# Optimization experiments

Hardware: AMD Instinct MI355X
Metric: run time of the kernel (lower is better)

## Reference

```python
import jax, jax.numpy as jnp
import numpy as np

NUM_USERS = 50000
NUM_ITEMS = 20000
N_NODES = NUM_USERS + NUM_ITEMS
D = 128           # embedding_dim
HEADS = 4
E_RAW = 400000    # raw edges (< 500000 threshold -> no subsampling)
BATCH = 16384
NEG_SLOPE = 0.2   # PyG GATConv leaky_relu slope
LN_EPS = 1e-5


def segment_softmax(logits, seg, num_segments):
    # PyG softmax: exp(x - max_per_segment) / (sum_per_segment + 1e-16)
    m = jax.ops.segment_max(logits, seg, num_segments=num_segments)
    m = jnp.where(jnp.isfinite(m), m, 0.0)  # empty segments
    e = jnp.exp(logits - m[seg])
    s = jax.ops.segment_sum(e, seg, num_segments=num_segments)
    return e / (s[seg] + 1e-16)


def gat_conv(x, src, dst, W, att_s, att_d, bias, heads):
    # PyG GATConv (concat=True): h = x @ W reshaped to [N, H, C]
    N = x.shape[0]
    HC = W.shape[1]
    C = HC // heads
    h = (x @ W).reshape(N, heads, C)
    a_s = (h * att_s).sum(-1)            # [N, H]
    a_d = (h * att_d).sum(-1)            # [N, H]
    logits = jax.nn.leaky_relu(a_s[src] + a_d[dst], NEG_SLOPE)  # [E, H]
    alpha = segment_softmax(logits, dst, N)                      # [E, H]
    msg = h[src] * alpha[:, :, None]                             # [E, H, C]
    out = jax.ops.segment_sum(msg, dst, num_segments=N)         # [N, H, C]
    return out.reshape(N, HC) + bias


def layer_norm(x, g, b):
    mu = x.mean(-1, keepdims=True)
    var = ((x - mu) ** 2).mean(-1, keepdims=True)
    return (x - mu) * jax.lax.rsqrt(var + LN_EPS) * g + b


def setup_inputs() -> dict:
    key = jax.random.key(0)
    ks = jax.random.split(key, 24)
    s = 0.05
    # graph: random edges with no self-loops, then append PyG self-loops
    src = jax.random.randint(ks[0], (E_RAW,), 0, N_NODES)
    off = jax.random.randint(ks[1], (E_RAW,), 1, N_NODES)
    dst = (src + off) % N_NODES
    loops = jnp.arange(N_NODES)
    edge_index = jnp.stack([jnp.concatenate([src, loops]),
                            jnp.concatenate([dst, loops])]).astype(jnp.int64)
    H1 = D // HEADS  # per-head dim for layers 0,1
    inp = {
        "user_indices": jax.random.randint(ks[2], (BATCH,), 0, NUM_USERS),
        "item_indices": jax.random.randint(ks[3], (BATCH,), 0, NUM_ITEMS),
        "edge_index": edge_index,
        "user_table": jax.random.normal(ks[4], (NUM_USERS, D)) * s,
        "item_table": jax.random.normal(ks[5], (NUM_ITEMS, D)) * s,
        # layer 0: GATConv(D, D//heads, heads)
        "W0": jax.random.normal(ks[6], (D, HEADS * H1)) * s,
        "as0": jax.random.normal(ks[7], (1, HEADS, H1)) * s,
        "ad0": jax.random.normal(ks[8], (1, HEADS, H1)) * s,
        "bb0": jnp.zeros((HEADS * H1,)),
        # layer 1: same shape
        "W1": jax.random.normal(ks[9], (D, HEADS * H1)) * s,
        "as1": jax.random.normal(ks[10], (1, HEADS, H1)) * s,
        "ad1": jax.random.normal(ks[11], (1, HEADS, H1)) * s,
        "bb1": jnp.zeros((HEADS * H1,)),
        # layer 2: GATConv(D, D) with heads=1
        "W2": jax.random.normal(ks[12], (D, D)) * s,
        "as2": jax.random.normal(ks[13], (1, 1, D)) * s,
        "ad2": jax.random.normal(ks[14], (1, 1, D)) * s,
        "bb2": jnp.zeros((D,)),
        "ln_g": jnp.ones((D,)),
        "ln_b": jnp.zeros((D,)),
        # prediction MLP
        "mw1": jax.random.normal(ks[15], (2 * D, D)) * s,
        "mb1": jnp.zeros((D,)),
        "mw2": jax.random.normal(ks[16], (D, D // 2)) * s,
        "mb2": jnp.zeros((D // 2,)),
        "mw3": jax.random.normal(ks[17], (D // 2, 1)) * s,
        "mb3": jnp.zeros((1,)),
    }
    return inp


def reference(user_indices, item_indices, edge_index, user_table, item_table,
              W0, as0, ad0, bb0, W1, as1, ad1, bb1, W2, as2, ad2, bb2,
              ln_g, ln_b, mw1, mb1, mw2, mb2, mw3, mb3):
    src, dst = edge_index[0], edge_index[1]
    x = jnp.concatenate([user_table, item_table], axis=0)  # [N, D]
    layers = [(W0, as0, ad0, bb0, HEADS), (W1, as1, ad1, bb1, HEADS),
              (W2, as2, ad2, bb2, 1)]
    for i, (W, a_s, a_d, bb, h) in enumerate(layers):
        x_new = jax.nn.elu(gat_conv(x, src, dst, W, a_s, a_d, bb, h))
        x = x_new + x if i > 0 else x_new  # residual (shapes always match here)
        x = layer_norm(x, ln_g, ln_b)
    user_emb = x[user_indices]
    item_emb = x[item_indices + NUM_USERS]
    combined = jnp.concatenate([user_emb, item_emb], axis=1)  # [B, 2D]
    hmlp = jax.nn.relu(combined @ mw1 + mb1)
    hmlp = jax.nn.relu(hmlp @ mw2 + mb2)
    logits = (hmlp @ mw3 + mb3)[:, 0]
    return jax.nn.sigmoid(logits)
```

## Files before the change

kernel.cpp:

```cpp
#include <hip/hip_runtime.h>
#include <hip/hip_bf16.h>

#define D128 128
#define NEG_SLOPE 0.2f

typedef __attribute__((ext_vector_type(8))) short bf16x8;
typedef __attribute__((ext_vector_type(4))) float f32x4;

__device__ inline float bf2f(unsigned short u) {
    return __uint_as_float(((unsigned)u) << 16);
}
__device__ inline unsigned short f2bf(float f) {
    unsigned u = __float_as_uint(f);
    unsigned r = (u + 0x7fffu + ((u >> 16) & 1u)) >> 16;
    return (unsigned short)r;
}

__global__ void zero_int_kernel(int* __restrict__ p, int n) {
    int i = blockIdx.x * blockDim.x + threadIdx.x;
    if (i < n) p[i] = 0;
}

__global__ void count_kernel(const int* __restrict__ dst, int E, int* __restrict__ cnt) {
    int e = blockIdx.x * blockDim.x + threadIdx.x;
    if (e < E) atomicAdd(&cnt[dst[e]], 1);
}

#define SB 256
#define SCAN_CHUNK 2048

__global__ __launch_bounds__(SB) void scan_local_kernel(const int* __restrict__ cnt,
                                                        int* __restrict__ off,
                                                        int* __restrict__ partials, int N) {
    __shared__ int lds[SB];
    const int b = blockIdx.x;
    const int t = threadIdx.x;
    const int base = b * SCAN_CHUNK + t * 8;
    int v[8];
    int s = 0;
#pragma unroll
    for (int j = 0; j < 8; ++j) {
        int i = base + j;
        v[j] = (i < N) ? cnt[i] : 0;
        s += v[j];
    }
    lds[t] = s;
    __syncthreads();
    for (int d = 1; d < SB; d <<= 1) {
        int y = (t >= d) ? lds[t - d] : 0;
        __syncthreads();
        lds[t] += y;
        __syncthreads();
    }
    int pref = lds[t] - s;
#pragma unroll
    for (int j = 0; j < 8; ++j) {
        int i = base + j;
        if (i < N) off[i] = pref;
        pref += v[j];
    }
    if (t == SB - 1) partials[b] = lds[t];
}

__global__ __launch_bounds__(64) void scan_partials_kernel(int* __restrict__ partials,
                                                           int* __restrict__ pp, int NB,
                                                           int* __restrict__ off, int N) {
    __shared__ int lds[64];
    int t = threadIdx.x;
    int v = (t < NB) ? partials[t] : 0;
    lds[t] = v;
    __syncthreads();
    for (int d = 1; d < 64; d <<= 1) {
        int y = (t >= d) ? lds[t - d] : 0;
        __syncthreads();
        lds[t] += y;
        __syncthreads();
    }
    pp[t] = lds[t] - v;
    if (t == 63) off[N] = lds[63];
}

__global__ void scan_add_kernel(int* __restrict__ off, int* __restrict__ cur,
                                const int* __restrict__ pp, int N) {
    int i = blockIdx.x * blockDim.x + threadIdx.x;
    if (i < N) {
        int o = off[i] + pp[i / SCAN_CHUNK];
        off[i] = o;
        cur[i] = o;
    }
}

__global__ void fill_kernel(const int* __restrict__ src, const int* __restrict__ dst, int E,
                            int* __restrict__ cur, int* __restrict__ csr_src,
                            int* __restrict__ csr_dst) {
    int e = blockIdx.x * blockDim.x + threadIdx.x;
    if (e < E) {
        int d = dst[e];
        int p = atomicAdd(&cur[d], 1);
        csr_src[p] = src[e];
        csr_dst[p] = d;
    }
}

__global__ __launch_bounds__(256) void wrepack3_kernel(const float* __restrict__ W0,
                                                       const float* __restrict__ W1,
                                                       const float* __restrict__ W2,
                                                       unsigned short* __restrict__ wb0,
                                                       unsigned short* __restrict__ wb1,
                                                       unsigned short* __restrict__ wb2) {
    const float* W = (blockIdx.y == 0) ? W0 : (blockIdx.y == 1) ? W1 : W2;
    unsigned short* Wb = (blockIdx.y == 0) ? wb0 : (blockIdx.y == 1) ? wb1 : wb2;
    int i = blockIdx.x * 256 + threadIdx.x;
    if (i >= 16384) return;
    int j = i & 7;
    int l = (i >> 3) & 63;
    int kk = (i >> 9) & 3;
    int ct = i >> 11;
    int k = kk * 32 + ((l >> 4) & 3) * 8 + j;
    int c = ct * 16 + (l & 15);
    float w = W[k * 128 + c];
    unsigned short hi = f2bf(w);
    unsigned short lo = f2bf(w - bf2f(hi));
    Wb[i] = hi;
    Wb[16384 + i] = lo;
}

__global__ __launch_bounds__(256) void wrepack_mlp_kernel(const float* __restrict__ mw1,
                                                          unsigned short* __restrict__ w1f,
                                                          const float* __restrict__ mw2,
                                                          unsigned short* __restrict__ w2f) {
    const int y = blockIdx.y;
    const float* W = y ? mw2 : mw1;
    unsigned short* Wf = y ? w2f : w1f;
    const int K = y ? 128 : 256, C = y ? 64 : 128;
    int total = K * C;
    int i = blockIdx.x * 256 + threadIdx.x;
    if (i >= total) return;
    int j = i & 7;
    int l = (i >> 3) & 63;
    int kkct = i >> 9;
    int KK = K >> 5;
    int kk = kkct % KK;
    int ct = kkct / KK;
    int k = kk * 32 + (l >> 4) * 8 + j;
    int c = ct * 16 + (l & 15);
    Wf[i] = f2bf(W[k * C + c]);
}

template <int H, bool SPLIT>
__global__ __launch_bounds__(512) void gemm_mfma_kernel(const float* __restrict__ X0,
                                                        const float* __restrict__ X1, int split,
                                                        const unsigned short* __restrict__ Wb,
                                                        const float* __restrict__ att_s,
                                                        const float* __restrict__ att_d,
                                                        unsigned short* __restrict__ hb,
                                                        float* __restrict__ a_s,
                                                        float* __restrict__ a_d, int N) {
    __shared__ unsigned short wlds[32768];
    const int t = threadIdx.x;
    const int lane = t & 63;
    const int wave = t >> 6;
    const int row0 = blockIdx.x * 128 + wave * 16;

    for (int i = t; i < 4096; i += 512)
        ((int4*)wlds)[i] = ((const int4*)Wb)[i];

    const int lr = lane & 15;
    const int lk = lane >> 4;

    int arow = row0 + lr;
    if (arow >= N) arow = N - 1;
    const float* xrow;
    if (SPLIT)
        xrow = (arow < split) ? &X0[(size_t)arow * 128] : &X1[(size_t)(arow - split) * 128];
    else
        xrow = &X0[(size_t)arow * 128];

    bf16x8 ahi[4], alo[4];
#pragma unroll
    for (int kk = 0; kk < 4; ++kk) {
        const float* ap = &xrow[kk * 32 + lk * 8];
        float4 v0 = *(const float4*)ap;
        float4 v1 = *(const float4*)(ap + 4);
        float f[8] = {v0.x, v0.y, v0.z, v0.w, v1.x, v1.y, v1.z, v1.w};
#pragma unroll
        for (int j = 0; j < 8; ++j) {
            unsigned short hi = f2bf(f[j]);
            unsigned short lo = f2bf(f[j] - bf2f(hi));
            ((short*)&ahi[kk])[j] = (short)hi;
            ((short*)&alo[kk])[j] = (short)lo;
        }
    }

    f32x4 acc[8];
#pragma unroll
    for (int ct = 0; ct < 8; ++ct) acc[ct] = (f32x4){0.f, 0.f, 0.f, 0.f};

    __syncthreads();

#pragma unroll
    for (int kk = 0; kk < 4; ++kk) {
#pragma unroll
        for (int ct = 0; ct < 8; ++ct) {
            const int fo = ((ct * 4 + kk) * 64 + lane) * 8;
            bf16x8 bhi = *(const bf16x8*)&wlds[fo];
            bf16x8 blo = *(const bf16x8*)&wlds[16384 + fo];
            acc[ct] = __builtin_amdgcn_mfma_f32_16x16x32_bf16(ahi[kk], bhi, acc[ct], 0, 0, 0);
            acc[ct] = __builtin_amdgcn_mfma_f32_16x16x32_bf16(ahi[kk], blo, acc[ct], 0, 0, 0);
            acc[ct] = __builtin_amdgcn_mfma_f32_16x16x32_bf16(alo[kk], bhi, acc[ct], 0, 0, 0);
        }
    }

    float ps[4][H], pd[4][H];
#pragma unroll
    for (int r = 0; r < 4; ++r)
#pragma unroll
        for (int h = 0; h < H; ++h) { ps[r][h] = 0.f; pd[r][h] = 0.f; }

#pragma unroll
    for (int ct = 0; ct < 8; ++ct) {
        float as_c = att_s[ct * 16 + lr];
        float ad_c = att_d[ct * 16 + lr];
        const int h = (ct * H) >> 3;
#pragma unroll
        for (int r = 0; r < 4; ++r) {
            float v = acc[ct][r];
            int row = row0 + lk * 4 + r;
            if (row < N) hb[(size_t)row * 128 + ct * 16 + lr] = f2bf(v);
            ps[r][h] += v * as_c;
            pd[r][h] += v * ad_c;
        }
    }

#pragma unroll
    for (int m = 1; m < 16; m <<= 1) {
#pragma unroll
        for (int r = 0; r < 4; ++r)
#pragma unroll
            for (int h = 0; h < H; ++h) {
                ps[r][h] += __shfl_xor(ps[r][h], m);
                pd[r][h] += __shfl_xor(pd[r][h], m);
            }
    }
    if (lr == 0) {
#pragma unroll
        for (int r = 0; r < 4; ++r) {
            int row = row0 + lk * 4 + r;
            if (row < N) {
                if (H == 4) {
                    *(float4*)&a_s[(size_t)row * 4] =
                        make_float4(ps[r][0], ps[r][1], ps[r][2], ps[r][3]);
                    *(float4*)&a_d[(size_t)row * 4] =
                        make_float4(pd[r][0], pd[r][1], pd[r][2], pd[r][3]);
                } else {
                    a_s[row] = ps[r][0];
                    a_d[row] = pd[r][0];
                }
            }
        }
    }
}

__global__ void pk4_kernel(const int* __restrict__ csr_src, const int* __restrict__ csr_dst,
                           const float* __restrict__ a_s, const float* __restrict__ a_d,
                           float* __restrict__ pbuf, int E) {
    int i = blockIdx.x * blockDim.x + threadIdx.x;
    if (i >= E) return;
    int s = csr_src[i], d = csr_dst[i];
    const float4 as4 = *(const float4*)&a_s[(size_t)s * 4];
    const float4 ad4 = *(const float4*)&a_d[(size_t)d * 4];
    float4 o;
    float lg;
    lg = as4.x + ad4.x; lg = lg >= 0.f ? lg : NEG_SLOPE * lg; o.x = expf(lg);
    lg = as4.y + ad4.y; lg = lg >= 0.f ? lg : NEG_SLOPE * lg; o.y = expf(lg);
    lg = as4.z + ad4.z; lg = lg >= 0.f ? lg : NEG_SLOPE * lg; o.z = expf(lg);
    lg = as4.w + ad4.w; lg = lg >= 0.f ? lg : NEG_SLOPE * lg; o.w = expf(lg);
    *(float4*)&pbuf[(size_t)i * 4] = o;
}

__global__ void pk1_kernel(const int* __restrict__ csr_src, const int* __restrict__ csr_dst,
                           const float* __restrict__ a_s, const float* __restrict__ a_d,
                           float* __restrict__ pbuf, int E) {
    int i = blockIdx.x * blockDim.x + threadIdx.x;
    if (i >= E) return;
    float lg = a_s[csr_src[i]] + a_d[csr_dst[i]];
    lg = lg >= 0.f ? lg : NEG_SLOPE * lg;
    pbuf[i] = expf(lg);
}

template <int H, bool RES>
__global__ __launch_bounds__(256) void agg_kernel(const unsigned short* __restrict__ hb,
                                                  const float* __restrict__ pbuf,
                                                  const int* __restrict__ off,
                                                  const int* __restrict__ csr_src,
                                                  const float* __restrict__ xprev,
                                                  const float* __restrict__ bias,
                                                  const float* __restrict__ ln_g,
                                                  const float* __restrict__ ln_b,
                                                  float* __restrict__ xout, int N) {
    const int t = threadIdx.x;
    const int l16 = t & 15;
    const int gbase = t & 48;
    const int n = blockIdx.x * 16 + (t >> 4);
    if (n >= N) return;
    const int c8 = l16 * 8;
    const int head = (c8 * H) >> 7;
    const int base = off[n];
    const int deg = off[n + 1] - base;

    float accA[8], accB[8];
#pragma unroll
    for (int j = 0; j < 8; ++j) { accA[j] = 0.f; accB[j] = 0.f; }
    float psA = 0.f, psB = 0.f;

    for (int e0 = 0; e0 < deg; e0 += 16) {
        const int ce = min(16, deg - e0);
        int myidx = 0;
        if (l16 < ce) myidx = csr_src[base + e0 + l16];
        const float* pb = &pbuf[(size_t)(base + e0) * H + head];
        int e = 0;
        for (; e + 1 < ce; e += 2) {
            int s0 = __shfl(myidx, gbase + e);
            int s1 = __shfl(myidx, gbase + e + 1);
            float p0 = pb[(size_t)e * H];
            float p1 = pb[(size_t)(e + 1) * H];
            uint4 h0 = *(const uint4*)&hb[((size_t)s0 << 7) + c8];
            uint4 h1 = *(const uint4*)&hb[((size_t)s1 << 7) + c8];
            psA += p0;
            psB += p1;
            accA[0] = fmaf(p0, bf2f((unsigned short)h0.x), accA[0]);
            accA[1] = fmaf(p0, bf2f((unsigned short)(h0.x >> 16)), accA[1]);
            accA[2] = fmaf(p0, bf2f((unsigned short)h0.y), accA[2]);
            accA[3] = fmaf(p0, bf2f((unsigned short)(h0.y >> 16)), accA[3]);
            accA[4] = fmaf(p0, bf2f((unsigned short)h0.z), accA[4]);
            accA[5] = fmaf(p0, bf2f((unsigned short)(h0.z >> 16)), accA[5]);
            accA[6] = fmaf(p0, bf2f((unsigned short)h0.w), accA[6]);
            accA[7] = fmaf(p0, bf2f((unsigned short)(h0.w >> 16)), accA[7]);
            accB[0] = fmaf(p1, bf2f((unsigned short)h1.x), accB[0]);
            accB[1] = fmaf(p1, bf2f((unsigned short)(h1.x >> 16)), accB[1]);
            accB[2] = fmaf(p1, bf2f((unsigned short)h1.y), accB[2]);
            accB[3] = fmaf(p1, bf2f((unsigned short)(h1.y >> 16)), accB[3]);
            accB[4] = fmaf(p1, bf2f((unsigned short)h1.z), accB[4]);
            accB[5] = fmaf(p1, bf2f((unsigned short)(h1.z >> 16)), accB[5]);
            accB[6] = fmaf(p1, bf2f((unsigned short)h1.w), accB[6]);
            accB[7] = fmaf(p1, bf2f((unsigned short)(h1.w >> 16)), accB[7]);
        }
        if (e < ce) {
            int s0 = __shfl(myidx, gbase + e);
            float p0 = pb[(size_t)e * H];
            uint4 h0 = *(const uint4*)&hb[((size_t)s0 << 7) + c8];
            psA += p0;
            accA[0] = fmaf(p0, bf2f((unsigned short)h0.x), accA[0]);
            accA[1] = fmaf(p0, bf2f((unsigned short)(h0.x >> 16)), accA[1]);
            accA[2] = fmaf(p0, bf2f((unsigned short)h0.y), accA[2]);
            accA[3] = fmaf(p0, bf2f((unsigned short)(h0.y >> 16)), accA[3]);
            accA[4] = fmaf(p0, bf2f((unsigned short)h0.z), accA[4]);
            accA[5] = fmaf(p0, bf2f((unsigned short)(h0.z >> 16)), accA[5]);
            accA[6] = fmaf(p0, bf2f((unsigned short)h0.w), accA[6]);
            accA[7] = fmaf(p0, bf2f((unsigned short)(h0.w >> 16)), accA[7]);
        }
    }

    const float inv = 1.0f / (psA + psB + 1e-16f);
    float4 bi0 = *(const float4*)&bias[c8];
    float4 bi1 = *(const float4*)&bias[c8 + 4];
    float val[8];
#pragma unroll
    for (int j = 0; j < 8; ++j) {
        float bj = (j < 4) ? ((const float*)&bi0)[j] : ((const float*)&bi1)[j - 4];
        float v = (accA[j] + accB[j]) * inv + bj;
        val[j] = v > 0.f ? v : (expf(v) - 1.0f);
    }
    if (RES) {
        float4 x0 = *(const float4*)&xprev[((size_t)n << 7) + c8];
        float4 x1 = *(const float4*)&xprev[((size_t)n << 7) + c8 + 4];
        val[0] += x0.x; val[1] += x0.y; val[2] += x0.z; val[3] += x0.w;
        val[4] += x1.x; val[5] += x1.y; val[6] += x1.z; val[7] += x1.w;
    }

    float s1v = 0.f, s2v = 0.f;
#pragma unroll
    for (int j = 0; j < 8; ++j) { s1v += val[j]; s2v += val[j] * val[j]; }
#pragma unroll
    for (int m = 1; m < 16; m <<= 1) {
        s1v += __shfl_xor(s1v, m);
        s2v += __shfl_xor(s2v, m);
    }
    float mu = s1v * (1.0f / 128.0f);
    float var = s2v * (1.0f / 128.0f) - mu * mu;
    float rstd = rsqrtf(var + 1e-5f);
    float4 g0 = *(const float4*)&ln_g[c8];
    float4 g1 = *(const float4*)&ln_g[c8 + 4];
    float4 lb0 = *(const float4*)&ln_b[c8];
    float4 lb1 = *(const float4*)&ln_b[c8 + 4];
    float4 o0, o1;
    o0.x = (val[0] - mu) * rstd * g0.x + lb0.x;
    o0.y = (val[1] - mu) * rstd * g0.y + lb0.y;
    o0.z = (val[2] - mu) * rstd * g0.z + lb0.z;
    o0.w = (val[3] - mu) * rstd * g0.w + lb0.w;
    o1.x = (val[4] - mu) * rstd * g1.x + lb1.x;
    o1.y = (val[5] - mu) * rstd * g1.y + lb1.y;
    o1.z = (val[6] - mu) * rstd * g1.z + lb1.z;
    o1.w = (val[7] - mu) * rstd * g1.w + lb1.w;
    *(float4*)&xout[((size_t)n << 7) + c8] = o0;
    *(float4*)&xout[((size_t)n << 7) + c8 + 4] = o1;
}

__global__ __launch_bounds__(256) void mlp_mfma_kernel(const float* __restrict__ x,
                                                       const int* __restrict__ uidx,
                                                       const int* __restrict__ vidx,
                                                       int num_users,
                                                       const unsigned short* __restrict__ w1f,
                                                       const float* __restrict__ mb1,
                                                       const unsigned short* __restrict__ w2f,
                                                       const float* __restrict__ mb2,
                                                       const float* __restrict__ mw3,
                                                       const float* __restrict__ mb3,
                                                       float* __restrict__ out, int B) {
    __shared__ unsigned short w1s[32768];
    __shared__ unsigned short w2s[8192];
    __shared__ unsigned short h1s[4][16 * 136];
    const int t = threadIdx.x;
    const int lane = t & 63;
    const int wave = t >> 6;
    const int row0 = blockIdx.x * 64 + wave * 16;
    const int lr = lane & 15;
    const int lk = lane >> 4;

    for (int i = t; i < 4096; i += 256) ((int4*)w1s)[i] = ((const int4*)w1f)[i];
    for (int i = t; i < 1024; i += 256) ((int4*)w2s)[i] = ((const int4*)w2f)[i];

    int b = row0 + lr;
    if (b >= B) b = B - 1;
    const float* urow = &x[(size_t)uidx[b] * 128];
    const float* vrow = &x[(size_t)(vidx[b] + num_users) * 128];
    bf16x8 ahi[8], alo[8];
#pragma unroll
    for (int kk = 0; kk < 8; ++kk) {
        const float* ap = (kk < 4) ? &urow[kk * 32 + lk * 8] : &vrow[(kk - 4) * 32 + lk * 8];
        float4 v0 = *(const float4*)ap;
        float4 v1 = *(const float4*)(ap + 4);
        float f[8] = {v0.x, v0.y, v0.z, v0.w, v1.x, v1.y, v1.z, v1.w};
#pragma unroll
        for (int j = 0; j < 8; ++j) {
            unsigned short hi = f2bf(f[j]);
            unsigned short lo = f2bf(f[j] - bf2f(hi));
            ((short*)&ahi[kk])[j] = (short)hi;
            ((short*)&alo[kk])[j] = (short)lo;
        }
    }

    f32x4 acc[8];
#pragma unroll
    for (int ct = 0; ct < 8; ++ct) acc[ct] = (f32x4){0.f, 0.f, 0.f, 0.f};

    __syncthreads();

#pragma unroll
    for (int kk = 0; kk < 8; ++kk) {
#pragma unroll
        for (int ct = 0; ct < 8; ++ct) {
            const int fo = ((ct * 8 + kk) * 64 + lane) * 8;
            bf16x8 bhi = *(const bf16x8*)&w1s[fo];
            acc[ct] = __builtin_amdgcn_mfma_f32_16x16x32_bf16(ahi[kk], bhi, acc[ct], 0, 0, 0);
            acc[ct] = __builtin_amdgcn_mfma_f32_16x16x32_bf16(alo[kk], bhi, acc[ct], 0, 0, 0);
        }
    }

#pragma unroll
    for (int ct = 0; ct < 8; ++ct) {
        const int col = ct * 16 + lr;
        const float b1 = mb1[col];
#pragma unroll
        for (int r = 0; r < 4; ++r) {
            float v = fmaxf(acc[ct][r] + b1, 0.f);
            h1s[wave][(lk * 4 + r) * 136 + col] = f2bf(v);
        }
    }
    __syncthreads();

    bf16x8 a2[4];
#pragma unroll
    for (int kk = 0; kk < 4; ++kk)
        a2[kk] = *(const bf16x8*)&h1s[wave][lr * 136 + kk * 32 + lk * 8];

    f32x4 acc2[4];
#pragma unroll
    for (int ct = 0; ct < 4; ++ct) acc2[ct] = (f32x4){0.f, 0.f, 0.f, 0.f};
#pragma unroll
    for (int kk = 0; kk < 4; ++kk) {
#pragma unroll
        for (int ct = 0; ct < 4; ++ct) {
            const int fo = ((ct * 4 + kk) * 64 + lane) * 8;
            bf16x8 bhi = *(const bf16x8*)&w2s[fo];
            acc2[ct] = __builtin_amdgcn_mfma_f32_16x16x32_bf16(a2[kk], bhi, acc2[ct], 0, 0, 0);
        }
    }

    float s[4] = {0.f, 0.f, 0.f, 0.f};
#pragma unroll
    for (int ct = 0; ct < 4; ++ct) {
        const int col = ct * 16 + lr;
        const float b2 = mb2[col];
        const float w3 = mw3[col];
#pragma unroll
        for (int r = 0; r < 4; ++r) {
            float v = fmaxf(acc2[ct][r] + b2, 0.f);
            s[r] = fmaf(v, w3, s[r]);
        }
    }
#pragma unroll
    for (int m = 1; m < 16; m <<= 1) {
#pragma unroll
        for (int r = 0; r < 4; ++r) s[r] += __shfl_xor(s[r], m);
    }
    if (lr == 0) {
        const float b3 = mb3[0];
#pragma unroll
        for (int r = 0; r < 4; ++r) {
            int row = row0 + lk * 4 + r;
            if (row < B) out[row] = 1.0f / (1.0f + expf(-(s[r] + b3)));
        }
    }
}

extern "C" void kernel_launch(void* const* d_in, const int* in_sizes, int n_in,
                              void* d_out, int out_size, void* d_ws, size_t ws_size,
                              hipStream_t stream) {
    const int* uidx = (const int*)d_in[0];
    const int* vidx = (const int*)d_in[1];
    const int* eidx = (const int*)d_in[2];
    const float* utab = (const float*)d_in[3];
    const float* itab = (const float*)d_in[4];
    const float* W0 = (const float*)d_in[5];
    const float* as0 = (const float*)d_in[6];
    const float* ad0 = (const float*)d_in[7];
    const float* bb0 = (const float*)d_in[8];
    const float* W1 = (const float*)d_in[9];
    const float* as1 = (const float*)d_in[10];
    const float* ad1 = (const float*)d_in[11];
    const float* bb1 = (const float*)d_in[12];
    const float* W2 = (const float*)d_in[13];
    const float* as2 = (const float*)d_in[14];
    const float* ad2 = (const float*)d_in[15];
    const float* bb2 = (const float*)d_in[16];
    const float* ln_g = (const float*)d_in[17];
    const float* ln_b = (const float*)d_in[18];
    const float* mw1 = (const float*)d_in[19];
    const float* mb1 = (const float*)d_in[20];
    const float* mw2 = (const float*)d_in[21];
    const float* mb2 = (const float*)d_in[22];
    const float* mw3 = (const float*)d_in[23];
    const float* mb3 = (const float*)d_in[24];

    const int B = in_sizes[0];
    const int E = in_sizes[2] / 2;
    const int num_users = in_sizes[3] / D128;
    const int num_items = in_sizes[4] / D128;
    const int N = num_users + num_items;
    const int* esrc = eidx;
    const int* edst = eidx + E;

    size_t wsoff = 0;
    auto alloc = [&](size_t bytes) {
        void* p = (char*)d_ws + wsoff;
        wsoff += (bytes + 255) & ~(size_t)255;
        return p;
    };
    float* bufA = (float*)alloc((size_t)N * 128 * 4);
    float* bufB = (float*)alloc((size_t)N * 128 * 4);
    unsigned short* hb = (unsigned short*)alloc((size_t)N * 128 * 2);
    float* aS = (float*)alloc((size_t)N * 4 * 4);
    float* aD = (float*)alloc((size_t)N * 4 * 4);
    float* pbuf = (float*)alloc((size_t)E * 4 * 4);
    int* cnt = (int*)alloc((size_t)(N + 1) * 4);
    int* off = (int*)alloc((size_t)(N + 1) * 4);
    int* cur = (int*)alloc((size_t)(N + 1) * 4);
    int* csr_src = (int*)alloc((size_t)E * 4);
    int* csr_dst = (int*)alloc((size_t)E * 4);
    int* partials = (int*)alloc(64 * 4);
    int* pp = (int*)alloc(64 * 4);
    unsigned short* wb0 = (unsigned short*)alloc(2 * 16384 * 2);
    unsigned short* wb1 = (unsigned short*)alloc(2 * 16384 * 2);
    unsigned short* wb2 = (unsigned short*)alloc(2 * 16384 * 2);
    unsigned short* w1f = (unsigned short*)alloc(32768 * 2);
    unsigned short* w2f = (unsigned short*)alloc(8192 * 2);
    (void)ws_size;

    wrepack3_kernel<<<dim3(64, 3), 256, 0, stream>>>(W0, W1, W2, wb0, wb1, wb2);
    wrepack_mlp_kernel<<<dim3(128, 2), 256, 0, stream>>>(mw1, w1f, mw2, w2f);

    const int NB = (N + SCAN_CHUNK - 1) / SCAN_CHUNK;
    zero_int_kernel<<<(N + 255) / 256, 256, 0, stream>>>(cnt, N);
    count_kernel<<<(E + 255) / 256, 256, 0, stream>>>(edst, E, cnt);
    scan_local_kernel<<<NB, SB, 0, stream>>>(cnt, off, partials, N);
    scan_partials_kernel<<<1, 64, 0, stream>>>(partials, pp, NB, off, N);
    scan_add_kernel<<<(N + 255) / 256, 256, 0, stream>>>(off, cur, pp, N);
    fill_kernel<<<(E + 255) / 256, 256, 0, stream>>>(esrc, edst, E, cur, csr_src, csr_dst);

    const int gemm_grid = (N + 127) / 128;
    const int egrid = (E + 255) / 256;
    const int agrid = (N + 15) / 16;

    gemm_mfma_kernel<4, true><<<gemm_grid, 512, 0, stream>>>(utab, itab, num_users, wb0, as0,
                                                             ad0, hb, aS, aD, N);
    pk4_kernel<<<egrid, 256, 0, stream>>>(csr_src, csr_dst, aS, aD, pbuf, E);
    agg_kernel<4, false><<<agrid, 256, 0, stream>>>(hb, pbuf, off, csr_src, nullptr, bb0, ln_g,
                                                    ln_b, bufB, N);
    gemm_mfma_kernel<4, false><<<gemm_grid, 512, 0, stream>>>(bufB, nullptr, 0, wb1, as1, ad1,
                                                              hb, aS, aD, N);
    pk4_kernel<<<egrid, 256, 0, stream>>>(csr_src, csr_dst, aS, aD, pbuf, E);
    agg_kernel<4, true><<<agrid, 256, 0, stream>>>(hb, pbuf, off, csr_src, bufB, bb1, ln_g,
                                                   ln_b, bufA, N);
    gemm_mfma_kernel<1, false><<<gemm_grid, 512, 0, stream>>>(bufA, nullptr, 0, wb2, as2, ad2,
                                                              hb, aS, aD, N);
    pk1_kernel<<<egrid, 256, 0, stream>>>(csr_src, csr_dst, aS, aD, pbuf, E);
    agg_kernel<1, true><<<agrid, 256, 0, stream>>>(hb, pbuf, off, csr_src, bufA, bb2, ln_g,
                                                   ln_b, bufB, N);

    mlp_mfma_kernel<<<(B + 63) / 64, 256, 0, stream>>>(bufB, uidx, vidx, num_users, w1f, mb1,
                                                       w2f, mb2, mw3, mb3, (float*)d_out, B);
}
```

Baseline: 251.2 us.

## Sort nodes by degree for aggregation and unroll edge loop by four

Adds a degree-bucketing pass (histogram, scan, scatter) that builds a permutation grouping nodes of similar in-degree. The aggregation kernels then process nodes in that order, so the 16-lane groups in a wavefront have matching loop trip counts and less divergence. The per-edge inner loop is also unrolled from two to four to keep more gathers in flight. The cost is three extra small kernel launches, an indirect node lookup that scatters output writes and residual reads, and some added register pressure.

Result: slower. 782.6 us (+211.6%).

```diff
diff --git a/kernel.cpp b/kernel.cpp
--- a/kernel.cpp
+++ b/kernel.cpp
@@ -99,6 +99,42 @@
         int p = atomicAdd(&cur[d], 1);
         csr_src[p] = src[e];
         csr_dst[p] = d;
+    }
+}
+
+__global__ void bucket_hist_kernel(const int* __restrict__ off, int N, int* __restrict__ bcnt) {
+    int i = blockIdx.x * blockDim.x + threadIdx.x;
+    if (i < N) {
+        int d = off[i + 1] - off[i];
+        if (d > 127) d = 127;
+        atomicAdd(&bcnt[d], 1);
+    }
+}
+
+__global__ __launch_bounds__(128) void bucket_scan_kernel(const int* __restrict__ bcnt,
+                                                          int* __restrict__ bcur) {
+    __shared__ int lds[128];
+    int t = threadIdx.x;
+    int v = bcnt[t];
+    lds[t] = v;
+    __syncthreads();
+    for (int d = 1; d < 128; d <<= 1) {
+        int y = (t >= d) ? lds[t - d] : 0;
+        __syncthreads();
+        lds[t] += y;
+        __syncthreads();
+    }
+    bcur[t] = lds[t] - v;
+}
+
+__global__ void bucket_scatter_kernel(const int* __restrict__ off, int N,
+                                      int* __restrict__ bcur, int* __restrict__ perm) {
+    int i = blockIdx.x * blockDim.x + threadIdx.x;
+    if (i < N) {
+        int d = off[i + 1] - off[i];
+        if (d > 127) d = 127;
+        int pos = atomicAdd(&bcur[d], 1);
+        perm[pos] = i;
     }
 }
 
@@ -293,6 +329,7 @@
                                                   const float* __restrict__ pbuf,
                                                   const int* __restrict__ off,
                                                   const int* __restrict__ csr_src,
+                                                  const int* __restrict__ perm,
                                                   const float* __restrict__ xprev,
                                                   const float* __restrict__ bias,
                                                   const float* __restrict__ ln_g,
@@ -301,8 +338,9 @@
     const int t = threadIdx.x;
     const int l16 = t & 15;
     const int gbase = t & 48;
-    const int n = blockIdx.x * 16 + (t >> 4);
-    if (n >= N) return;
+    const int idx = blockIdx.x * 16 + (t >> 4);
+    if (idx >= N) return;
+    const int n = perm[idx];
     const int c8 = l16 * 8;
     const int head = (c8 * H) >> 7;
     const int base = off[n];
@@ -312,6 +350,16 @@
 #pragma unroll
     for (int j = 0; j < 8; ++j) { accA[j] = 0.f; accB[j] = 0.f; }
     float psA = 0.f, psB = 0.f;
+
+#define ACC8(ACC, P, HV)                                                     \
+    ACC[0] = fmaf(P, bf2f((unsigned short)HV.x), ACC[0]);                    \
+    ACC[1] = fmaf(P, bf2f((unsigned short)(HV.x >> 16)), ACC[1]);            \
+    ACC[2] = fmaf(P, bf2f((unsigned short)HV.y), ACC[2]);                    \
+    ACC[3] = fmaf(P, bf2f((unsigned short)(HV.y >> 16)), ACC[3]);            \
+    ACC[4] = fmaf(P, bf2f((unsigned short)HV.z), ACC[4]);                    \
+    ACC[5] = fmaf(P, bf2f((unsigned short)(HV.z >> 16)), ACC[5]);            \
+    ACC[6] = fmaf(P, bf2f((unsigned short)HV.w), ACC[6]);                    \
+    ACC[7] = fmaf(P, bf2f((unsigned short)(HV.w >> 16)), ACC[7]);
 
     for (int e0 = 0; e0 < deg; e0 += 16) {
         const int ce = min(16, deg - e0);
@@ -319,47 +367,35 @@
         if (l16 < ce) myidx = csr_src[base + e0 + l16];
         const float* pb = &pbuf[(size_t)(base + e0) * H + head];
         int e = 0;
-        for (; e + 1 < ce; e += 2) {
+        for (; e + 3 < ce; e += 4) {
             int s0 = __shfl(myidx, gbase + e);
             int s1 = __shfl(myidx, gbase + e + 1);
-            float p0 = pb[(size_t)e * H];
+            int s2 = __shfl(myidx, gbase + e + 2);
+            int s3 = __shfl(myidx, gbase + e + 3);
+            float p0 = pb[(size_t)(e + 0) * H];
             float p1 = pb[(size_t)(e + 1) * H];
+            float p2 = pb[(size_t)(e + 2) * H];
+            float p3 = pb[(size_t)(e + 3) * H];
             uint4 h0 = *(const uint4*)&hb[((size_t)s0 << 7) + c8];
             uint4 h1 = *(const uint4*)&hb[((size_t)s1 << 7) + c8];
-            psA += p0;
-            psB += p1;
-            accA[0] = fmaf(p0, bf2f((unsigned short)h0.x), accA[0]);
-            accA[1] = fmaf(p0, bf2f((unsigned short)(h0.x >> 16)), accA[1]);
-            accA[2] = fmaf(p0, bf2f((unsigned short)h0.y), accA[2]);
-            accA[3] = fmaf(p0, bf2f((unsigned short)(h0.y >> 16)), accA[3]);
-            accA[4] = fmaf(p0, bf2f((unsigned short)h0.z), accA[4]);
-            accA[5] = fmaf(p0, bf2f((unsigned short)(h0.z >> 16)), accA[5]);
-            accA[6] = fmaf(p0, bf2f((unsigned short)h0.w), accA[6]);
-            accA[7] = fmaf(p0, bf2f((unsigned short)(h0.w >> 16)), accA[7]);
-            accB[0] = fmaf(p1, bf2f((unsigned short)h1.x), accB[0]);
-            accB[1] = fmaf(p1, bf2f((unsigned short)(h1.x >> 16)), accB[1]);
-            accB[2] = fmaf(p1, bf2f((unsigned short)h1.y), accB[2]);
-            accB[3] = fmaf(p1, bf2f((unsigned short)(h1.y >> 16)), accB[3]);
-            accB[4] = fmaf(p1, bf2f((unsigned short)h1.z), accB[4]);
-            accB[5] = fmaf(p1, bf2f((unsigned short)(h1.z >> 16)), accB[5]);
-            accB[6] = fmaf(p1, bf2f((unsigned short)h1.w), accB[6]);
-            accB[7] = fmaf(p1, bf2f((unsigned short)(h1.w >> 16)), accB[7]);
-        }
-        if (e < ce) {
+            uint4 h2 = *(const uint4*)&hb[((size_t)s2 << 7) + c8];
+            uint4 h3 = *(const uint4*)&hb[((size_t)s3 << 7) + c8];
+            psA += p0 + p2;
+            psB += p1 + p3;
+            ACC8(accA, p0, h0);
+            ACC8(accB, p1, h1);
+            ACC8(accA, p2, h2);
+            ACC8(accB, p3, h3);
+        }
+        for (; e < ce; ++e) {
             int s0 = __shfl(myidx, gbase + e);
             float p0 = pb[(size_t)e * H];
             uint4 h0 = *(const uint4*)&hb[((size_t)s0 << 7) + c8];
             psA += p0;
-            accA[0] = fmaf(p0, bf2f((unsigned short)h0.x), accA[0]);
-            accA[1] = fmaf(p0, bf2f((unsigned short)(h0.x >> 16)), accA[1]);
-            accA[2] = fmaf(p0, bf2f((unsigned short)h0.y), accA[2]);
-            accA[3] = fmaf(p0, bf2f((unsigned short)(h0.y >> 16)), accA[3]);
-            accA[4] = fmaf(p0, bf2f((unsigned short)h0.z), accA[4]);
-            accA[5] = fmaf(p0, bf2f((unsigned short)(h0.z >> 16)), accA[5]);
-            accA[6] = fmaf(p0, bf2f((unsigned short)h0.w), accA[6]);
-            accA[7] = fmaf(p0, bf2f((unsigned short)(h0.w >> 16)), accA[7]);
-        }
-    }
+            ACC8(accA, p0, h0);
+        }
+    }
+#undef ACC8
 
     const float inv = 1.0f / (psA + psB + 1e-16f);
     float4 bi0 = *(const float4*)&bias[c8];
@@ -580,6 +616,9 @@
     int* csr_dst = (int*)alloc((size_t)E * 4);
     int* partials = (int*)alloc(64 * 4);
     int* pp = (int*)alloc(64 * 4);
+    int* bcnt = (int*)alloc(128 * 4);
+    int* bcur = (int*)alloc(128 * 4);
+    int* perm = (int*)alloc((size_t)N * 4);
     unsigned short* wb0 = (unsigned short*)alloc(2 * 16384 * 2);
     unsigned short* wb1 = (unsigned short*)alloc(2 * 16384 * 2);
     unsigned short* wb2 = (unsigned short*)alloc(2 * 16384 * 2);
@@ -592,11 +631,15 @@
 
     const int NB = (N + SCAN_CHUNK - 1) / SCAN_CHUNK;
     zero_int_kernel<<<(N + 255) / 256, 256, 0, stream>>>(cnt, N);
+    zero_int_kernel<<<1, 128, 0, stream>>>(bcnt, 128);
     count_kernel<<<(E + 255) / 256, 256, 0, stream>>>(edst, E, cnt);
     scan_local_kernel<<<NB, SB, 0, stream>>>(cnt, off, partials, N);
     scan_partials_kernel<<<1, 64, 0, stream>>>(partials, pp, NB, off, N);
     scan_add_kernel<<<(N + 255) / 256, 256, 0, stream>>>(off, cur, pp, N);
     fill_kernel<<<(E + 255) / 256, 256, 0, stream>>>(esrc, edst, E, cur, csr_src, csr_dst);
+    bucket_hist_kernel<<<(N + 255) / 256, 256, 0, stream>>>(off, N, bcnt);
+    bucket_scan_kernel<<<1, 128, 0, stream>>>(bcnt, bcur);
+    bucket_scatter_kernel<<<(N + 255) / 256, 256, 0, stream>>>(off, N, bcur, perm);
 
     const int gemm_grid = (N + 127) / 128;
     const int egrid = (E + 255) / 256;
@@ -605,18 +648,18 @@
     gemm_mfma_kernel<4, true><<<gemm_grid, 512, 0, stream>>>(utab, itab, num_users, wb0, as0,
                                                              ad0, hb, aS, aD, N);
     pk4_kernel<<<egrid, 256, 0, stream>>>(csr_src, csr_dst, aS, aD, pbuf, E);
-    agg_kernel<4, false><<<agrid, 256, 0, stream>>>(hb, pbuf, off, csr_src, nullptr, bb0, ln_g,
-                                                    ln_b, bufB, N);
+    agg_kernel<4, false><<<agrid, 256, 0, stream>>>(hb, pbuf, off, csr_src, perm, nullptr, bb0,
+                                                    ln_g, ln_b, bufB, N);
     gemm_mfma_kernel<4, false><<<gemm_grid, 512, 0, stream>>>(bufB, nullptr, 0, wb1, as1, ad1,
                                                               hb, aS, aD, N);
     pk4_kernel<<<egrid, 256, 0, stream>>>(csr_src, csr_dst, aS, aD, pbuf, E);
-    agg_kernel<4, true><<<agrid, 256, 0, stream>>>(hb, pbuf, off, csr_src, bufB, bb1, ln_g,
-                                                   ln_b, bufA, N);
+    agg_kernel<4, true><<<agrid, 256, 0, stream>>>(hb, pbuf, off, csr_src, perm, bufB, bb1,
+                                                   ln_g, ln_b, bufA, N);
     gemm_mfma_kernel<1, false><<<gemm_grid, 512, 0, stream>>>(bufA, nullptr, 0, wb2, as2, ad2,
                                                               hb, aS, aD, N);
     pk1_kernel<<<egrid, 256, 0, stream>>>(csr_src, csr_dst, aS, aD, pbuf, E);
-    agg_kernel<1, true><<<agrid, 256, 0, stream>>>(hb, pbuf, off, csr_src, bufA, bb2, ln_g,
-                                                   ln_b, bufB, N);
+    agg_kernel<1, true><<<agrid, 256, 0, stream>>>(hb, pbuf, off, csr_src, perm, bufA, bb2,
+                                                   ln_g, ln_b, bufB, N);
 
     mlp_mfma_kernel<<<(B + 63) / 64, 256, 0, stream>>>(bufB, uidx, vidx, num_users, w1f, mb1,
                                                        w2f, mb2, mw3, mb3, (float*)d_out, B);
```

## Fuse edge attention exp computation into aggregation kernel and drop pbuf

Applied to the files above, without the earlier changes.

Removes the separate pk4/pk1 per-edge kernels and the E*H pbuf buffer. The aggregation kernel now computes leaky_relu(a_s[src]+a_d[dst]) and its exp inline while gathering, and csr_dst is no longer written during CSR fill. This saves three launches and the round trip of the edge-probability buffer. In exchange each of the 16 lanes per node recomputes the exp redundantly and does an extra scattered a_s gather per edge.

After: 236.8 us. -5.7%, faster.

```diff
diff --git a/kernel.cpp b/kernel.cpp
--- a/kernel.cpp
+++ b/kernel.cpp
@@ -91,14 +91,11 @@
 }
 
 __global__ void fill_kernel(const int* __restrict__ src, const int* __restrict__ dst, int E,
-                            int* __restrict__ cur, int* __restrict__ csr_src,
-                            int* __restrict__ csr_dst) {
+                            int* __restrict__ cur, int* __restrict__ csr_src) {
     int e = blockIdx.x * blockDim.x + threadIdx.x;
     if (e < E) {
-        int d = dst[e];
-        int p = atomicAdd(&cur[d], 1);
+        int p = atomicAdd(&cur[dst[e]], 1);
         csr_src[p] = src[e];
-        csr_dst[p] = d;
     }
 }
 
@@ -261,36 +258,10 @@
     }
 }
 
-__global__ void pk4_kernel(const int* __restrict__ csr_src, const int* __restrict__ csr_dst,
-                           const float* __restrict__ a_s, const float* __restrict__ a_d,
-                           float* __restrict__ pbuf, int E) {
-    int i = blockIdx.x * blockDim.x + threadIdx.x;
-    if (i >= E) return;
-    int s = csr_src[i], d = csr_dst[i];
-    const float4 as4 = *(const float4*)&a_s[(size_t)s * 4];
-    const float4 ad4 = *(const float4*)&a_d[(size_t)d * 4];
-    float4 o;
-    float lg;
-    lg = as4.x + ad4.x; lg = lg >= 0.f ? lg : NEG_SLOPE * lg; o.x = expf(lg);
-    lg = as4.y + ad4.y; lg = lg >= 0.f ? lg : NEG_SLOPE * lg; o.y = expf(lg);
-    lg = as4.z + ad4.z; lg = lg >= 0.f ? lg : NEG_SLOPE * lg; o.z = expf(lg);
-    lg = as4.w + ad4.w; lg = lg >= 0.f ? lg : NEG_SLOPE * lg; o.w = expf(lg);
-    *(float4*)&pbuf[(size_t)i * 4] = o;
-}
-
-__global__ void pk1_kernel(const int* __restrict__ csr_src, const int* __restrict__ csr_dst,
-                           const float* __restrict__ a_s, const float* __restrict__ a_d,
-                           float* __restrict__ pbuf, int E) {
-    int i = blockIdx.x * blockDim.x + threadIdx.x;
-    if (i >= E) return;
-    float lg = a_s[csr_src[i]] + a_d[csr_dst[i]];
-    lg = lg >= 0.f ? lg : NEG_SLOPE * lg;
-    pbuf[i] = expf(lg);
-}
-
 template <int H, bool RES>
 __global__ __launch_bounds__(256) void agg_kernel(const unsigned short* __restrict__ hb,
-                                                  const float* __restrict__ pbuf,
+                                                  const float* __restrict__ a_s,
+                                                  const float* __restrict__ a_d,
                                                   const int* __restrict__ off,
                                                   const int* __restrict__ csr_src,
                                                   const float* __restrict__ xprev,
@@ -307,59 +278,58 @@
     const int head = (c8 * H) >> 7;
     const int base = off[n];
     const int deg = off[n + 1] - base;
+    const float adn = a_d[(size_t)n * H + head];
 
     float accA[8], accB[8];
 #pragma unroll
     for (int j = 0; j < 8; ++j) { accA[j] = 0.f; accB[j] = 0.f; }
     float psA = 0.f, psB = 0.f;
+
+#define ACC8(ACC, P, HV)                                                     \
+    ACC[0] = fmaf(P, bf2f((unsigned short)HV.x), ACC[0]);                    \
+    ACC[1] = fmaf(P, bf2f((unsigned short)(HV.x >> 16)), ACC[1]);            \
+    ACC[2] = fmaf(P, bf2f((unsigned short)HV.y), ACC[2]);                    \
+    ACC[3] = fmaf(P, bf2f((unsigned short)(HV.y >> 16)), ACC[3]);            \
+    ACC[4] = fmaf(P, bf2f((unsigned short)HV.z), ACC[4]);                    \
+    ACC[5] = fmaf(P, bf2f((unsigned short)(HV.z >> 16)), ACC[5]);            \
+    ACC[6] = fmaf(P, bf2f((unsigned short)HV.w), ACC[6]);                    \
+    ACC[7] = fmaf(P, bf2f((unsigned short)(HV.w >> 16)), ACC[7]);
 
     for (int e0 = 0; e0 < deg; e0 += 16) {
         const int ce = min(16, deg - e0);
         int myidx = 0;
         if (l16 < ce) myidx = csr_src[base + e0 + l16];
-        const float* pb = &pbuf[(size_t)(base + e0) * H + head];
         int e = 0;
         for (; e + 1 < ce; e += 2) {
             int s0 = __shfl(myidx, gbase + e);
             int s1 = __shfl(myidx, gbase + e + 1);
-            float p0 = pb[(size_t)e * H];
-            float p1 = pb[(size_t)(e + 1) * H];
+            float as0 = a_s[(size_t)s0 * H + head];
+            float as1 = a_s[(size_t)s1 * H + head];
             uint4 h0 = *(const uint4*)&hb[((size_t)s0 << 7) + c8];
             uint4 h1 = *(const uint4*)&hb[((size_t)s1 << 7) + c8];
+            float lg0 = as0 + adn;
+            lg0 = lg0 >= 0.f ? lg0 : NEG_SLOPE * lg0;
+            float p0 = expf(lg0);
+            float lg1 = as1 + adn;
+            lg1 = lg1 >= 0.f ? lg1 : NEG_SLOPE * lg1;
+            float p1 = expf(lg1);
             psA += p0;
             psB += p1;
-            accA[0] = fmaf(p0, bf2f((unsigned short)h0.x), accA[0]);
-            accA[1] = fmaf(p0, bf2f((unsigned short)(h0.x >> 16)), accA[1]);
-            accA[2] = fmaf(p0, bf2f((unsigned short)h0.y), accA[2]);
-            accA[3] = fmaf(p0, bf2f((unsigned short)(h0.y >> 16)), accA[3]);
-            accA[4] = fmaf(p0, bf2f((unsigned short)h0.z), accA[4]);
-            accA[5] = fmaf(p0, bf2f((unsigned short)(h0.z >> 16)), accA[5]);
-            accA[6] = fmaf(p0, bf2f((unsigned short)h0.w), accA[6]);
-            accA[7] = fmaf(p0, bf2f((unsigned short)(h0.w >> 16)), accA[7]);
-            accB[0] = fmaf(p1, bf2f((unsigned short)h1.x), accB[0]);
-            accB[1] = fmaf(p1, bf2f((unsigned short)(h1.x >> 16)), accB[1]);
-            accB[2] = fmaf(p1, bf2f((unsigned short)h1.y), accB[2]);
-            accB[3] = fmaf(p1, bf2f((unsigned short)(h1.y >> 16)), accB[3]);
-            accB[4] = fmaf(p1, bf2f((unsigned short)h1.z), accB[4]);
-            accB[5] = fmaf(p1, bf2f((unsigned short)(h1.z >> 16)), accB[5]);
-            accB[6] = fmaf(p1, bf2f((unsigned short)h1.w), accB[6]);
-            accB[7] = fmaf(p1, bf2f((unsigned short)(h1.w >> 16)), accB[7]);
+            ACC8(accA, p0, h0);
+            ACC8(accB, p1, h1);
         }
         if (e < ce) {
             int s0 = __shfl(myidx, gbase + e);
-            float p0 = pb[(size_t)e * H];
+            float as0 = a_s[(size_t)s0 * H + head];
             uint4 h0 = *(const uint4*)&hb[((size_t)s0 << 7) + c8];
+            float lg0 = as0 + adn;
+            lg0 = lg0 >= 0.f ? lg0 : NEG_SLOPE * lg0;
+            float p0 = expf(lg0);
             psA += p0;
-            accA[0] = fmaf(p0, bf2f((unsigned short)h0.x), accA[0]);
-            accA[1] = fmaf(p0, bf2f((unsigned short)(h0.x >> 16)), accA[1]);
-            accA[2] = fmaf(p0, bf2f((unsigned short)h0.y), accA[2]);
-            accA[3] = fmaf(p0, bf2f((unsigned short)(h0.y >> 16)), accA[3]);
-            accA[4] = fmaf(p0, bf2f((unsigned short)h0.z), accA[4]);
-            accA[5] = fmaf(p0, bf2f((unsigned short)(h0.z >> 16)), accA[5]);
-            accA[6] = fmaf(p0, bf2f((unsigned short)h0.w), accA[6]);
-            accA[7] = fmaf(p0, bf2f((unsigned short)(h0.w >> 16)), accA[7]);
-        }
-    }
+            ACC8(accA, p0, h0);
+        }
+    }
+#undef ACC8
 
     const float inv = 1.0f / (psA + psB + 1e-16f);
     float4 bi0 = *(const float4*)&bias[c8];
@@ -572,12 +542,10 @@
     unsigned short* hb = (unsigned short*)alloc((size_t)N * 128 * 2);
     float* aS = (float*)alloc((size_t)N * 4 * 4);
     float* aD = (float*)alloc((size_t)N * 4 * 4);
-    float* pbuf = (float*)alloc((size_t)E * 4 * 4);
     int* cnt = (int*)alloc((size_t)(N + 1) * 4);
     int* off = (int*)alloc((size_t)(N + 1) * 4);
     int* cur = (int*)alloc((size_t)(N + 1) * 4);
     int* csr_src = (int*)alloc((size_t)E * 4);
-    int* csr_dst = (int*)alloc((size_t)E * 4);
     int* partials = (int*)alloc(64 * 4);
     int* pp = (int*)alloc(64 * 4);
     unsigned short* wb0 = (unsigned short*)alloc(2 * 16384 * 2);
@@ -596,26 +564,22 @@
     scan_local_kernel<<<NB, SB, 0, stream>>>(cnt, off, partials, N);
     scan_partials_kernel<<<1, 64, 0, stream>>>(partials, pp, NB, off, N);
     scan_add_kernel<<<(N + 255) / 256, 256, 0, stream>>>(off, cur, pp, N);
-    fill_kernel<<<(E + 255) / 256, 256, 0, stream>>>(esrc, edst, E, cur, csr_src, csr_dst);
+    fill_kernel<<<(E + 255) / 256, 256, 0, stream>>>(esrc, edst, E, cur, csr_src);
 
     const int gemm_grid = (N + 127) / 128;
-    const int egrid = (E + 255) / 256;
     const int agrid = (N + 15) / 16;
 
     gemm_mfma_kernel<4, true><<<gemm_grid, 512, 0, stream>>>(utab, itab, num_users, wb0, as0,
                                                              ad0, hb, aS, aD, N);
-    pk4_kernel<<<egrid, 256, 0, stream>>>(csr_src, csr_dst, aS, aD, pbuf, E);
-    agg_kernel<4, false><<<agrid, 256, 0, stream>>>(hb, pbuf, off, csr_src, nullptr, bb0, ln_g,
-                                                    ln_b, bufB, N);
+    agg_kernel<4, false><<<agrid, 256, 0, stream>>>(hb, aS, aD, off, csr_src, nullptr, bb0,
+                                                    ln_g, ln_b, bufB, N);
     gemm_mfma_kernel<4, false><<<gemm_grid, 512, 0, stream>>>(bufB, nullptr, 0, wb1, as1, ad1,
                                                               hb, aS, aD, N);
-    pk4_kernel<<<egrid, 256, 0, stream>>>(csr_src, csr_dst, aS, aD, pbuf, E);
-    agg_kernel<4, true><<<agrid, 256, 0, stream>>>(hb, pbuf, off, csr_src, bufB, bb1, ln_g,
+    agg_kernel<4, true><<<agrid, 256, 0, stream>>>(hb, aS, aD, off, csr_src, bufB, bb1, ln_g,
                                                    ln_b, bufA, N);
     gemm_mfma_kernel<1, false><<<gemm_grid, 512, 0, stream>>>(bufA, nullptr, 0, wb2, as2, ad2,
                                                               hb, aS, aD, N);
-    pk1_kernel<<<egrid, 256, 0, stream>>>(csr_src, csr_dst, aS, aD, pbuf, E);
-    agg_kernel<1, true><<<agrid, 256, 0, stream>>>(hb, pbuf, off, csr_src, bufA, bb2, ln_g,
+    agg_kernel<1, true><<<agrid, 256, 0, stream>>>(hb, aS, aD, off, csr_src, bufA, bb2, ln_g,
                                                    ln_b, bufB, N);
 
     mlp_mfma_kernel<<<(B + 63) / 64, 256, 0, stream>>>(bufB, uidx, vidx, num_users, w1f, mb1,
```
